# Kernel optimization log

Measured on AMD Instinct MI355X. Metric: run time of the kernel, lower is better.

Reference implementation:

```python
import jax, jax.numpy as jnp
import numpy as np

B, H, L, E, MODES = 32, 8, 4096, 64, 64


def setup_inputs() -> dict:
    key = jax.random.key(0)
    kx, kw, ki = jax.random.split(key, 3)
    x = jax.random.normal(kx, (B, H, L, E), dtype=jnp.float32)
    # nn.Parameter(torch.randn(E, E, modes, 2) / sqrt(E))
    weights = jax.random.normal(kw, (E, E, MODES, 2), dtype=jnp.float32) / np.sqrt(E)
    # register_buffer: sorted random permutation of [0, seq_len//2) truncated to modes (unique)
    index = jnp.sort(jax.random.permutation(ki, L // 2)[:MODES]).astype(jnp.int64)
    return {"x": x, "weights": weights, "index": index}


def reference(x, weights, index):
    # x: [B, H, L, E]
    Bs, Hs, Ls, Es = x.shape
    xt = jnp.swapaxes(x, -1, -2)                 # [B, H, E, L]
    x_ft = jnp.fft.rfft(xt, axis=-1)             # [B, H, E, L//2+1] complex64
    w_c = weights[..., 0] + 1j * weights[..., 1]  # [E, E, modes] complex
    sel = x_ft[..., index]                       # gather selected modes: [B, H, E, modes]
    out_sel = jnp.einsum('bhei,eoi->bhoi', sel, w_c)  # [B, H, E_out, modes]
    out_ft = jnp.zeros_like(x_ft).at[..., index].set(out_sel)  # scatter into zero spectrum
    y = jnp.fft.irfft(out_ft, n=Ls, axis=-1)     # [B, H, E, L]
    return jnp.swapaxes(y, -1, -2)               # [B, H, L, E]
```

## Files before the change

kernel.cpp:

```cpp
#include <hip/hip_runtime.h>
#include <hip/hip_bf16.h>
#include <math.h>

#define LTOT   4096
#define EDIM   64
#define NMODES 64
#define BH     256
#define TWO_PI 6.28318530717958647692f

typedef float f32x4 __attribute__((ext_vector_type(4)));
typedef short s16x8 __attribute__((ext_vector_type(8)));

__device__ inline unsigned short f2bf(float f) {
    unsigned u = __builtin_bit_cast(unsigned, f);
    u += 0x7fff + ((u >> 16) & 1);
    return (unsigned short)(u >> 16);
}
__device__ inline unsigned packbf(float lo, float hi) {
    return (unsigned)f2bf(lo) | ((unsigned)f2bf(hi) << 16);
}

__global__ void k_tab_m(const int* __restrict__ index, unsigned short* __restrict__ Tm) {
    int k = blockIdx.x;
    int f = index[k];
    for (int l = threadIdx.x; l < LTOT; l += blockDim.x) {
        int m = (f * l) & (LTOT - 1);
        float th = (float)m * (TWO_PI / (float)LTOT);
        float s, c; sincosf(th, &s, &c);
        Tm[(size_t)(2 * k) * LTOT + l]     = f2bf(c);
        Tm[(size_t)(2 * k + 1) * LTOT + l] = f2bf(-s);
    }
}
__global__ void k_tab_t(const int* __restrict__ index, unsigned short* __restrict__ Tt) {
    int l = blockIdx.x * 4 + (threadIdx.x >> 6);
    int k = threadIdx.x & 63;
    int f = index[k];
    int m = (f * l) & (LTOT - 1);
    float th = (float)m * (TWO_PI / (float)LTOT);
    float s, c; sincosf(th, &s, &c);
    ((unsigned*)Tt)[l * 64 + k] = packbf(c, s);
}

#define S1PITCH 72
__global__ __launch_bounds__(256) void k_stage1(const float* __restrict__ x,
                                                const unsigned short* __restrict__ Tm,
                                                float* __restrict__ Xp) {
    int bh = blockIdx.x >> 2, part = blockIdx.x & 3;
    const float* xb = x + (size_t)bh * LTOT * EDIM;
    __shared__ unsigned xT[64 * (S1PITCH / 2)];

    int t = threadIdx.x;
    int q = t & 15, lp = t >> 4;
    int lane = t & 63, wave = t >> 6;
    int r = lane & 15, kb8 = lane >> 4;
    int wbase = wave * 32;

    f32x4 acc[4][2];
    #pragma unroll
    for (int i = 0; i < 4; ++i) { acc[i][0] = (f32x4)0.f; acc[i][1] = (f32x4)0.f; }

    for (int tile = 0; tile < 16; ++tile) {
        int l0 = part * 1024 + tile * 64;
        __syncthreads();
        const float* b0 = xb + (size_t)(l0 + 2 * lp) * EDIM + 4 * q;
        float4 a0 = *(const float4*)(b0);
        float4 a1 = *(const float4*)(b0 + EDIM);
        float4 a2 = *(const float4*)(b0 + 32 * EDIM);
        float4 a3 = *(const float4*)(b0 + 33 * EDIM);
        float A0[4] = {a0.x, a0.y, a0.z, a0.w};
        float A1[4] = {a1.x, a1.y, a1.z, a1.w};
        float A2[4] = {a2.x, a2.y, a2.z, a2.w};
        float A3[4] = {a3.x, a3.y, a3.z, a3.w};
        #pragma unroll
        for (int j = 0; j < 4; ++j) {
            int e = 4 * q + j;
            xT[e * (S1PITCH / 2) + lp]      = packbf(A0[j], A1[j]);
            xT[e * (S1PITCH / 2) + lp + 16] = packbf(A2[j], A3[j]);
        }
        __syncthreads();
        #pragma unroll
        for (int kk = 0; kk < 2; ++kk) {
            s16x8 bf[2];
            #pragma unroll
            for (int ns = 0; ns < 2; ++ns) {
                int m = wbase + ns * 16 + r;
                bf[ns] = *(const s16x8*)(Tm + (size_t)m * LTOT + (l0 + kk * 32 + kb8 * 8));
            }
            #pragma unroll
            for (int es = 0; es < 4; ++es) {
                int e = es * 16 + r;
                s16x8 af = *(const s16x8*)((const unsigned short*)xT + e * S1PITCH + kk * 32 + kb8 * 8);
                #pragma unroll
                for (int ns = 0; ns < 2; ++ns)
                    acc[es][ns] = __builtin_amdgcn_mfma_f32_16x16x32_bf16(af, bf[ns], acc[es][ns], 0, 0, 0);
            }
        }
    }
    float* Xb = Xp + ((size_t)part * BH + bh) * (64 * 128);
    #pragma unroll
    for (int es = 0; es < 4; ++es)
        #pragma unroll
        for (int ns = 0; ns < 2; ++ns)
            #pragma unroll
            for (int g = 0; g < 4; ++g) {
                int e = es * 16 + kb8 * 4 + g;
                int m = wbase + ns * 16 + r;
                Xb[e * 128 + m] = acc[es][ns][g];
            }
}

__global__ __launch_bounds__(512) void k_stage2(const float* __restrict__ Xp,
                                                const float2* __restrict__ w2,
                                                const int* __restrict__ index,
                                                unsigned short* __restrict__ AB) {
    int bh0 = blockIdx.x * 2;
    __shared__ float Xs[2][64 * 128];
    int t = threadIdx.x;

    #pragma unroll
    for (int bhi = 0; bhi < 2; ++bhi) {
        f32x4 a[4];
        #pragma unroll
        for (int i = 0; i < 4; ++i) a[i] = (f32x4)0.f;
        #pragma unroll
        for (int p = 0; p < 4; ++p) {
            const f32x4* src = (const f32x4*)(Xp + ((size_t)p * BH + bh0 + bhi) * 8192);
            #pragma unroll
            for (int i = 0; i < 4; ++i) a[i] += src[t + i * 512];
        }
        f32x4* dst = (f32x4*)Xs[bhi];
        #pragma unroll
        for (int i = 0; i < 4; ++i) dst[t + i * 512] = a[i];
    }
    __syncthreads();

    int k = t & 63, og = t >> 6;
    int f = index[k];
    float cc = (f == 0 ? 1.0f : 2.0f) / (float)LTOT;
    float aR[2][8] = {}, aI[2][8] = {};
    for (int e = 0; e < 64; ++e) {
        float2 X0 = *(const float2*)&Xs[0][e * 128 + 2 * k];
        float2 X1 = *(const float2*)&Xs[1][e * 128 + 2 * k];
        #pragma unroll
        for (int oi = 0; oi < 8; ++oi) {
            int o = og * 8 + oi;
            float2 wv = w2[((size_t)e * 64 + o) * 64 + k];
            aR[0][oi] += X0.x * wv.x - X0.y * wv.y;
            aI[0][oi] += X0.x * wv.y + X0.y * wv.x;
            aR[1][oi] += X1.x * wv.x - X1.y * wv.y;
            aI[1][oi] += X1.x * wv.y + X1.y * wv.x;
        }
    }
    #pragma unroll
    for (int bhi = 0; bhi < 2; ++bhi)
        #pragma unroll
        for (int oi = 0; oi < 8; ++oi) {
            int o = og * 8 + oi;
            size_t b = ((size_t)(bh0 + bhi) * 128 + 2 * k) * 64 + o;
            AB[b]      = f2bf(cc * aR[bhi][oi]);
            AB[b + 64] = (f == 0) ? (unsigned short)0 : f2bf(-cc * aI[bhi][oi]);
        }
}

#define S3PITCH 72
__global__ __launch_bounds__(256) void k_stage3(const unsigned short* __restrict__ Tt,
                                                const unsigned short* __restrict__ AB,
                                                float* __restrict__ y) {
    int bh = blockIdx.x >> 2, qtr = blockIdx.x & 3;
    __shared__ unsigned short ABl[128 * S3PITCH];
    int t = threadIdx.x;
    int lane = t & 63, wave = t >> 6;
    int r = lane & 15, kb8 = lane >> 4;

    {
        const unsigned* src = (const unsigned*)(AB + (size_t)bh * 8192);
        #pragma unroll
        for (int i = 0; i < 16; ++i) {
            int idx = t + i * 256;
            int m = idx >> 5, op = idx & 31;
            ((unsigned*)ABl)[m * (S3PITCH / 2) + op] = src[idx];
        }
    }
    __syncthreads();

    s16x8 bfr[4][4];
    #pragma unroll
    for (int ks = 0; ks < 4; ++ks)
        #pragma unroll
        for (int ns = 0; ns < 4; ++ns) {
            s16x8 v;
            #pragma unroll
            for (int i = 0; i < 8; ++i) {
                int m = ks * 32 + kb8 * 8 + i;
                v[i] = (short)ABl[m * S3PITCH + ns * 16 + r];
            }
            bfr[ks][ns] = v;
        }

    for (int it = 0; it < 16; ++it) {
        int lbase = qtr * 1024 + it * 64 + wave * 16;
        s16x8 af[4];
        #pragma unroll
        for (int ks = 0; ks < 4; ++ks)
            af[ks] = *(const s16x8*)(Tt + (size_t)(lbase + r) * 128 + ks * 32 + kb8 * 8);
        f32x4 acc[4];
        #pragma unroll
        for (int ns = 0; ns < 4; ++ns) acc[ns] = (f32x4)0.f;
        #pragma unroll
        for (int ks = 0; ks < 4; ++ks)
            #pragma unroll
            for (int ns = 0; ns < 4; ++ns)
                acc[ns] = __builtin_amdgcn_mfma_f32_16x16x32_bf16(af[ks], bfr[ks][ns], acc[ns], 0, 0, 0);
        float* yb = y + ((size_t)bh * LTOT + lbase) * EDIM;
        #pragma unroll
        for (int ns = 0; ns < 4; ++ns)
            #pragma unroll
            for (int g = 0; g < 4; ++g)
                yb[(kb8 * 4 + g) * EDIM + ns * 16 + r] = acc[ns][g];
    }
}

extern "C" void kernel_launch(void* const* d_in, const int* in_sizes, int n_in,
                              void* d_out, int out_size, void* d_ws, size_t ws_size,
                              hipStream_t stream) {
    const float* x     = (const float*)d_in[0];
    const float* w     = (const float*)d_in[1];
    const int*   index = (const int*)d_in[2];
    float* y  = (float*)d_out;
    float* ws = (float*)d_ws;

    unsigned short* Tm = (unsigned short*)ws;
    unsigned short* Tt = (unsigned short*)(ws + 262144);
    float*          Xp = ws + 524288;
    unsigned short* AB = (unsigned short*)(ws + 8912896);

    hipLaunchKernelGGL(k_tab_m,  dim3(NMODES), dim3(256), 0, stream, index, Tm);
    hipLaunchKernelGGL(k_tab_t,  dim3(1024),   dim3(256), 0, stream, index, Tt);
    hipLaunchKernelGGL(k_stage1, dim3(BH * 4), dim3(256), 0, stream, x, Tm, Xp);
    hipLaunchKernelGGL(k_stage2, dim3(BH / 2), dim3(512), 0, stream, Xp, (const float2*)w, index, AB);
    hipLaunchKernelGGL(k_stage3, dim3(BH * 4), dim3(256), 0, stream, Tt, AB, y);
}
```

Before: 203.1 us.

## Swizzle stage1 LDS, retile stage1 waves, transpose stage3 GEMM for vector stores

```diff
diff --git a/kernel.cpp b/kernel.cpp
--- a/kernel.cpp
+++ b/kernel.cpp
@@ -17,7 +17,11 @@
     return (unsigned short)(u >> 16);
 }
 __device__ inline unsigned packbf(float lo, float hi) {
-    return (unsigned)f2bf(lo) | ((unsigned)f2bf(hi) << 16);
+    float2 t; t.x = lo; t.y = hi;
+    __hip_bfloat162 h = __float22bfloat162_rn(t);
+    unsigned r;
+    __builtin_memcpy(&r, &h, 4);
+    return r;
 }
 
 __global__ void k_tab_m(const int* __restrict__ index, unsigned short* __restrict__ Tm) {
@@ -41,23 +45,26 @@
     ((unsigned*)Tt)[l * 64 + k] = packbf(c, s);
 }
 
-#define S1PITCH 72
+#define S1P32 36
 __global__ __launch_bounds__(256) void k_stage1(const float* __restrict__ x,
                                                 const unsigned short* __restrict__ Tm,
                                                 float* __restrict__ Xp) {
     int bh = blockIdx.x >> 2, part = blockIdx.x & 3;
     const float* xb = x + (size_t)bh * LTOT * EDIM;
-    __shared__ unsigned xT[64 * (S1PITCH / 2)];
+    __shared__ unsigned xT[64 * S1P32];
 
     int t = threadIdx.x;
     int q = t & 15, lp = t >> 4;
     int lane = t & 63, wave = t >> 6;
     int r = lane & 15, kb8 = lane >> 4;
-    int wbase = wave * 32;
-
-    f32x4 acc[4][2];
-    #pragma unroll
-    for (int i = 0; i < 4; ++i) { acc[i][0] = (f32x4)0.f; acc[i][1] = (f32x4)0.f; }
+    int esb = (wave & 1) * 2;
+    int mb  = (wave >> 1) * 64;
+
+    f32x4 acc[2][4];
+    #pragma unroll
+    for (int i = 0; i < 2; ++i)
+        #pragma unroll
+        for (int n = 0; n < 4; ++n) acc[i][n] = (f32x4)0.f;
 
     for (int tile = 0; tile < 16; ++tile) {
         int l0 = part * 1024 + tile * 64;
@@ -74,37 +81,40 @@
         #pragma unroll
         for (int j = 0; j < 4; ++j) {
             int e = 4 * q + j;
-            xT[e * (S1PITCH / 2) + lp]      = packbf(A0[j], A1[j]);
-            xT[e * (S1PITCH / 2) + lp + 16] = packbf(A2[j], A3[j]);
+            unsigned v = ((unsigned)(e >> 2) & 7u) << 2;
+            xT[e * S1P32 + (( (unsigned)lp      ) ^ v)] = packbf(A0[j], A1[j]);
+            xT[e * S1P32 + (( (unsigned)lp + 16u) ^ v)] = packbf(A2[j], A3[j]);
         }
         __syncthreads();
         #pragma unroll
         for (int kk = 0; kk < 2; ++kk) {
-            s16x8 bf[2];
-            #pragma unroll
-            for (int ns = 0; ns < 2; ++ns) {
-                int m = wbase + ns * 16 + r;
+            s16x8 bf[4];
+            #pragma unroll
+            for (int ns = 0; ns < 4; ++ns) {
+                int m = mb + ns * 16 + r;
                 bf[ns] = *(const s16x8*)(Tm + (size_t)m * LTOT + (l0 + kk * 32 + kb8 * 8));
             }
             #pragma unroll
-            for (int es = 0; es < 4; ++es) {
-                int e = es * 16 + r;
-                s16x8 af = *(const s16x8*)((const unsigned short*)xT + e * S1PITCH + kk * 32 + kb8 * 8);
+            for (int es = 0; es < 2; ++es) {
+                int e = (esb + es) * 16 + r;
+                unsigned v = ((unsigned)(e >> 2) & 7u) << 2;
+                const unsigned* rowp = xT + e * S1P32;
+                s16x8 af = *(const s16x8*)(rowp + (((unsigned)(kk * 16 + kb8 * 4)) ^ v));
                 #pragma unroll
-                for (int ns = 0; ns < 2; ++ns)
+                for (int ns = 0; ns < 4; ++ns)
                     acc[es][ns] = __builtin_amdgcn_mfma_f32_16x16x32_bf16(af, bf[ns], acc[es][ns], 0, 0, 0);
             }
         }
     }
     float* Xb = Xp + ((size_t)part * BH + bh) * (64 * 128);
     #pragma unroll
-    for (int es = 0; es < 4; ++es)
-        #pragma unroll
-        for (int ns = 0; ns < 2; ++ns)
+    for (int es = 0; es < 2; ++es)
+        #pragma unroll
+        for (int ns = 0; ns < 4; ++ns)
             #pragma unroll
             for (int g = 0; g < 4; ++g) {
-                int e = es * 16 + kb8 * 4 + g;
-                int m = wbase + ns * 16 + r;
+                int e = (esb + es) * 16 + kb8 * 4 + g;
+                int m = mb + ns * 16 + r;
                 Xb[e * 128 + m] = acc[es][ns][g];
             }
 }
@@ -112,7 +122,7 @@
 __global__ __launch_bounds__(512) void k_stage2(const float* __restrict__ Xp,
                                                 const float2* __restrict__ w2,
                                                 const int* __restrict__ index,
-                                                unsigned short* __restrict__ AB) {
+                                                unsigned* __restrict__ ABo) {
     int bh0 = blockIdx.x * 2;
     __shared__ float Xs[2][64 * 128];
     int t = threadIdx.x;
@@ -156,67 +166,58 @@
         #pragma unroll
         for (int oi = 0; oi < 8; ++oi) {
             int o = og * 8 + oi;
-            size_t b = ((size_t)(bh0 + bhi) * 128 + 2 * k) * 64 + o;
-            AB[b]      = f2bf(cc * aR[bhi][oi]);
-            AB[b + 64] = (f == 0) ? (unsigned short)0 : f2bf(-cc * aI[bhi][oi]);
-        }
-}
-
-#define S3PITCH 72
+            float im = (f == 0) ? 0.0f : -cc * aI[bhi][oi];
+            ABo[((size_t)(bh0 + bhi) * 64 + o) * 64 + k] = packbf(cc * aR[bhi][oi], im);
+        }
+}
+
+#define S3P16 136
 __global__ __launch_bounds__(256) void k_stage3(const unsigned short* __restrict__ Tt,
-                                                const unsigned short* __restrict__ AB,
+                                                const unsigned* __restrict__ ABo,
                                                 float* __restrict__ y) {
     int bh = blockIdx.x >> 2, qtr = blockIdx.x & 3;
-    __shared__ unsigned short ABl[128 * S3PITCH];
+    __shared__ unsigned short ABl[64 * S3P16];
     int t = threadIdx.x;
     int lane = t & 63, wave = t >> 6;
     int r = lane & 15, kb8 = lane >> 4;
 
     {
-        const unsigned* src = (const unsigned*)(AB + (size_t)bh * 8192);
+        const unsigned* src = ABo + (size_t)bh * 4096;
+        unsigned* dst = (unsigned*)ABl;
         #pragma unroll
         for (int i = 0; i < 16; ++i) {
             int idx = t + i * 256;
-            int m = idx >> 5, op = idx & 31;
-            ((unsigned*)ABl)[m * (S3PITCH / 2) + op] = src[idx];
+            int o = idx >> 6, c = idx & 63;
+            dst[o * (S3P16 / 2) + c] = src[idx];
         }
     }
     __syncthreads();
 
-    s16x8 bfr[4][4];
-    #pragma unroll
-    for (int ks = 0; ks < 4; ++ks)
-        #pragma unroll
-        for (int ns = 0; ns < 4; ++ns) {
-            s16x8 v;
-            #pragma unroll
-            for (int i = 0; i < 8; ++i) {
-                int m = ks * 32 + kb8 * 8 + i;
-                v[i] = (short)ABl[m * S3PITCH + ns * 16 + r];
-            }
-            bfr[ks][ns] = v;
-        }
+    s16x8 afr[4][4];
+    #pragma unroll
+    for (int es = 0; es < 4; ++es)
+        #pragma unroll
+        for (int ks = 0; ks < 4; ++ks)
+            afr[es][ks] = *(const s16x8*)(ABl + (es * 16 + r) * S3P16 + ks * 32 + kb8 * 8);
 
     for (int it = 0; it < 16; ++it) {
-        int lbase = qtr * 1024 + it * 64 + wave * 16;
-        s16x8 af[4];
+        int ltile = qtr * 1024 + it * 64 + wave * 16;
+        s16x8 btf[4];
         #pragma unroll
         for (int ks = 0; ks < 4; ++ks)
-            af[ks] = *(const s16x8*)(Tt + (size_t)(lbase + r) * 128 + ks * 32 + kb8 * 8);
+            btf[ks] = *(const s16x8*)(Tt + (size_t)(ltile + r) * 128 + ks * 32 + kb8 * 8);
         f32x4 acc[4];
         #pragma unroll
-        for (int ns = 0; ns < 4; ++ns) acc[ns] = (f32x4)0.f;
+        for (int es = 0; es < 4; ++es) acc[es] = (f32x4)0.f;
         #pragma unroll
         for (int ks = 0; ks < 4; ++ks)
             #pragma unroll
-            for (int ns = 0; ns < 4; ++ns)
-                acc[ns] = __builtin_amdgcn_mfma_f32_16x16x32_bf16(af[ks], bfr[ks][ns], acc[ns], 0, 0, 0);
-        float* yb = y + ((size_t)bh * LTOT + lbase) * EDIM;
-        #pragma unroll
-        for (int ns = 0; ns < 4; ++ns)
-            #pragma unroll
-            for (int g = 0; g < 4; ++g)
-                yb[(kb8 * 4 + g) * EDIM + ns * 16 + r] = acc[ns][g];
+            for (int es = 0; es < 4; ++es)
+                acc[es] = __builtin_amdgcn_mfma_f32_16x16x32_bf16(afr[es][ks], btf[ks], acc[es], 0, 0, 0);
+        float* yb = y + ((size_t)bh * LTOT + ltile + r) * EDIM;
+        #pragma unroll
+        for (int es = 0; es < 4; ++es)
+            *(f32x4*)(yb + es * 16 + kb8 * 4) = acc[es];
     }
 }
 
@@ -232,11 +233,11 @@
     unsigned short* Tm = (unsigned short*)ws;
     unsigned short* Tt = (unsigned short*)(ws + 262144);
     float*          Xp = ws + 524288;
-    unsigned short* AB = (unsigned short*)(ws + 8912896);
+    unsigned*       ABo = (unsigned*)(ws + 8912896);
 
     hipLaunchKernelGGL(k_tab_m,  dim3(NMODES), dim3(256), 0, stream, index, Tm);
     hipLaunchKernelGGL(k_tab_t,  dim3(1024),   dim3(256), 0, stream, index, Tt);
     hipLaunchKernelGGL(k_stage1, dim3(BH * 4), dim3(256), 0, stream, x, Tm, Xp);
-    hipLaunchKernelGGL(k_stage2, dim3(BH / 2), dim3(512), 0, stream, Xp, (const float2*)w, index, AB);
-    hipLaunchKernelGGL(k_stage3, dim3(BH * 4), dim3(256), 0, stream, Tt, AB, y);
-}
+    hipLaunchKernelGGL(k_stage2, dim3(BH / 2), dim3(512), 0, stream, Xp, (const float2*)w, index, ABo);
+    hipLaunchKernelGGL(k_stage3, dim3(BH * 4), dim3(256), 0, stream, Tt, ABo, y);
+}
```

Result: slower. 210.4 us (+3.6%).
